# Kernel optimization log

Hardware: AMD Instinct MI355X
Metric: run time of the kernel (lower is better)

The kernel has to match this reference:

```python
import jax, jax.numpy as jnp
import numpy as np
from jax import lax

B, T_PAST, T_FUT, F_IN, F_OUT, H = 512, 128, 48, 64, 16, 512


def setup_inputs() -> dict:
    key = jax.random.key(0)
    ks = jax.random.split(key, 12)
    s = jnp.float32(0.05)
    p = lambda k, shape: jax.random.normal(k, shape, jnp.float32) * s
    return {
        "inp": jax.random.normal(ks[0], (B, T_PAST, F_IN), jnp.float32),
        "target_seq": jax.random.normal(ks[1], (B, T_FUT, F_OUT), jnp.float32),
        "enc1_Wk": p(ks[2], (F_IN, 4 * H)), "enc1_Wr": p(ks[3], (H, 4 * H)), "enc1_b": jnp.zeros((4 * H,), jnp.float32),
        "enc2_Wk": p(ks[4], (H, 4 * H)), "enc2_Wr": p(ks[5], (H, 4 * H)), "enc2_b": jnp.zeros((4 * H,), jnp.float32),
        "dec1_Wk": p(ks[6], (F_OUT, 4 * H)), "dec1_Wr": p(ks[7], (H, 4 * H)), "dec1_b": jnp.zeros((4 * H,), jnp.float32),
        "dec2_Wk": p(ks[8], (H, 4 * H)), "dec2_Wr": p(ks[9], (H, 4 * H)), "dec2_b": jnp.zeros((4 * H,), jnp.float32),
        "fc_W": p(ks[10], (H, F_OUT)), "fc_b": jnp.zeros((F_OUT,), jnp.float32),
    }


def _gates(z, c_prev):
    # Keras gate order: i, f, g(cell), o
    i, f, g, o = jnp.split(z, 4, axis=-1)
    c = jax.nn.sigmoid(f) * c_prev + jax.nn.sigmoid(i) * jnp.tanh(g)
    h = jax.nn.sigmoid(o) * jnp.tanh(c)
    return h, c


def _lstm_layer(xs, h0, c0, Wk, Wr, b):
    # xs: (B, T, D) -> (hs (B,T,H), hT, cT)
    xz = jnp.einsum("btd,dg->btg", xs, Wk) + b  # input projection precomputed
    def step(carry, xz_t):
        h, c = carry
        h2, c2 = _gates(xz_t + h @ Wr, c)
        return (h2, c2), h2
    (hT, cT), hs = lax.scan(step, (h0, c0), jnp.swapaxes(xz, 0, 1))
    return jnp.swapaxes(hs, 0, 1), hT, cT


def reference(inp, target_seq,
              enc1_Wk, enc1_Wr, enc1_b, enc2_Wk, enc2_Wr, enc2_b,
              dec1_Wk, dec1_Wr, dec1_b, dec2_Wk, dec2_Wr, dec2_b,
              fc_W, fc_b):
    b = inp.shape[0]
    z = jnp.zeros((b, H), inp.dtype)
    # Encoder: layer2 initial state = layer1 final state (as in source)
    h1s, h1, c1 = _lstm_layer(inp, z, z, enc1_Wk, enc1_Wr, enc1_b)
    _, h2, c2 = _lstm_layer(h1s, h1, c1, enc2_Wk, enc2_Wr, enc2_b)
    # Decoder: every future step restarts from (h2, c2) with teacher-forced
    # inputs -> steps are independent, compute all in parallel.
    z1 = (jnp.einsum("btf,fg->btg", target_seq, dec1_Wk)
          + (h2 @ dec1_Wr)[:, None, :] + dec1_b)          # (B, Tf, 4H)
    h1d, c1d = _gates(z1, c2[:, None, :])
    # layer2: input = h1d, initial state = (h1d, c1d) (chained per source)
    z2 = jnp.einsum("bth,hg->btg", h1d, dec2_Wk + dec2_Wr) + dec2_b
    h2d, _ = _gates(z2, c1d)
    return jnp.einsum("bth,hf->btf", h2d, fc_W) + fc_b    # (B, Tf, F_OUT)
```

## Files before the change

### kernel.cpp

```cpp
#include <hip/hip_runtime.h>


typedef _Float16 f16;
typedef _Float16 h8 __attribute__((ext_vector_type(8)));
typedef _Float16 h4 __attribute__((ext_vector_type(4)));
typedef float f32x4 __attribute__((ext_vector_type(4)));
typedef unsigned long long ull;

#define DEV static __device__ __forceinline__

constexpr int NB   = 512;
constexpr int TP   = 128;
constexpr int TFU  = 48;
constexpr int FIN  = 64;
constexpr int FOUT = 16;
constexpr int HS   = 512;
constexpr int G4   = 2048;

DEV float sigf(float x) { return 1.0f / (1.0f + __expf(-x)); }
DEV float tanh_(float x) { float e = __expf(2.0f * x); return 1.0f - 2.0f / (e + 1.0f); }

DEV void issue_ld(h8& d, const f16* p) {
  asm volatile("global_load_dwordx4 %0, %1, off" : "=v"(d) : "v"(p));
}
DEV void issue_ldc(h8& d, const f16* p) {
  asm volatile("global_load_dwordx4 %0, %1, off sc0 sc1" : "=v"(d) : "v"(p));
}
#define ILDX(dst, base, B) \
  asm volatile("global_load_dwordx4 %0, %1, off offset:" #B : "=v"(dst) : "v"(base));
#define ASM_VM0    asm volatile("s_waitcnt vmcnt(0)" ::: "memory")
#define ASM_VMC(N) asm volatile("s_waitcnt vmcnt(" #N ")" ::: "memory")
#define SBAR       __builtin_amdgcn_sched_barrier(0)

DEV void st_coh_h4(f16* p, h4 v) {
  union { h4 h; ull u; } c;
  c.h = v;
  __hip_atomic_store((ull*)p, c.u, __ATOMIC_RELAXED, __HIP_MEMORY_SCOPE_AGENT);
}

DEV unsigned xcc_id() {
  unsigned x;
  asm("s_getreg_b32 %0, hwreg(HW_REG_XCC_ID)" : "=s"(x));
  return x & 7;
}

DEV int ic2zc(int ic) { return ((ic >> 4) & 3) * 512 + ((ic >> 6) << 4) + (ic & 15); }

__global__ void k_conv(const float* __restrict__ a, const float* __restrict__ b,
                       f16* __restrict__ a16, f16* __restrict__ b16) {
  const size_t NA = (size_t)NB * TP * FIN;
  const size_t NBT = (size_t)NB * TFU * FOUT;
  for (size_t i = (size_t)blockIdx.x * blockDim.x + threadIdx.x; i < NA + NBT;
       i += (size_t)gridDim.x * blockDim.x) {
    if (i < NA) a16[i] = (f16)a[i];
    else        b16[i - NA] = (f16)b[i - NA];
  }
}

__global__ void k_bias(const float* __restrict__ b1, const float* __restrict__ b2,
                       const float* __restrict__ b3, const float* __restrict__ b4,
                       float* __restrict__ o1, float* __restrict__ o2,
                       float* __restrict__ o3, float* __restrict__ o4) {
  int ic = blockIdx.x * blockDim.x + threadIdx.x;
  if (ic < G4) {
    int zc = ic2zc(ic);
    o1[ic] = b1[zc]; o2[ic] = b2[zc]; o3[ic] = b3[zc]; o4[ic] = b4[zc];
  }
}

__global__ void k_pack(const float* __restrict__ A, const float* __restrict__ Bs,
                       int split, int NKC, int mode, f16* __restrict__ dst) {
  int i = blockIdx.x * blockDim.x + threadIdx.x;
  int total = 128 * NKC * 64;
  if (i >= total) return;
  int lane = i & 63, rem = i >> 6;
  int kc = rem % NKC, nt = rem / NKC;
  int zc = ic2zc(nt * 16 + (lane & 15));
  int k0 = kc * 32 + ((lane >> 4) << 3);
  h8 v;
#pragma unroll
  for (int j = 0; j < 8; j++) {
    int k = k0 + j;
    float x;
    if (mode == 2) x = A[(size_t)k * G4 + zc] + Bs[(size_t)k * G4 + zc];
    else x = (k < split) ? A[(size_t)k * G4 + zc] : Bs[(size_t)(k - split) * G4 + zc];
    v[j] = (f16)x;
  }
  *(h8*)(dst + (size_t)i * 8) = v;
}

__global__ void k_pack_dk16(const float* __restrict__ W, f16* __restrict__ dst) {
  int i = blockIdx.x * blockDim.x + threadIdx.x;
  if (i >= 128 * 64) return;
  int lane = i & 63, nt = i >> 6;
  int zc = ic2zc(nt * 16 + (lane & 15));
  h4 v;
#pragma unroll
  for (int j = 0; j < 4; j++) v[j] = (f16)W[(size_t)(((lane >> 4) << 2) + j) * G4 + zc];
  *(h4*)(dst + (size_t)i * 4) = v;
}

__global__ void k_pack_fc(const float* __restrict__ W, f16* __restrict__ dst) {
  int i = blockIdx.x * blockDim.x + threadIdx.x;
  if (i >= 32 * 64) return;
  int lane = i & 63, q = i >> 6;
  h4 v;
#pragma unroll
  for (int j = 0; j < 4; j++) {
    int k = q * 16 + ((lane >> 4) << 2) + j;
    v[j] = (f16)W[(size_t)k * FOUT + (lane & 15)];
  }
  *(h4*)(dst + (size_t)i * 4) = v;
}

template <int L, bool HIST>
__global__ __launch_bounds__(256, 1) void k_enc(
    const f16* __restrict__ wfrag, const float* __restrict__ biasI,
    f16* __restrict__ h1s, f16* __restrict__ h2r, f16* __restrict__ h2s,
    float* __restrict__ cT, const float* __restrict__ cInit,
    const f16* __restrict__ inp16, unsigned int* __restrict__ flags,
    int* __restrict__ roster) {
  constexpr int XKC = (L == 1) ? 2 : 16;
  constexpr int NKC = XKC + 16;
  constexpr size_t SLOT = (size_t)NB * HS;
  constexpr bool PLAIN_H = (L == 1) || HIST;

  extern __shared__ __align__(16) char smem[];
  f16* Bl = (f16*)smem;
  float* zl = (float*)(smem + (size_t)NKC * 4096);
  __shared__ int s_gc[2];

  const int tid = threadIdx.x, lane = tid & 63, wid = tid >> 6;
  const int wr = wid & 1, wc = wid >> 1;

  if (tid == 0) {
    unsigned x = xcc_id();
    int slot = atomicAdd(&roster[x], 1) & 31;
    s_gc[0] = (int)x; s_gc[1] = slot;
  }
  __syncthreads();
  const int g = s_gc[0], c = s_gc[1];
  const int b0 = g * 64;
  const int l15 = lane & 15, lk = (lane >> 4) << 3;
  const int trow = tid >> 2, tcol = (tid & 3) << 2;
  const int fbase = g * 32;

  {
    const uint4* src = (const uint4*)wfrag + (size_t)c * NKC * 256;
    uint4* dst = (uint4*)smem;
    for (int i = tid; i < NKC * 256; i += 256) dst[i] = src[i];
  }

  float bs[4][4];
#pragma unroll
  for (int ga = 0; ga < 4; ga++) {
    f32x4 bv = *(const f32x4*)(biasI + 64 * c + 16 * ga + tcol);
#pragma unroll
    for (int jj = 0; jj < 4; jj++) bs[ga][jj] = bv[jj];
  }

  float cst[4];
  if (L == 1) {
    cst[0] = cst[1] = cst[2] = cst[3] = 0.0f;
  } else {
    f32x4 cv = *(const f32x4*)(cInit + (size_t)(b0 + trow) * HS + 16 * c + tcol);
#pragma unroll
    for (int jj = 0; jj < 4; jj++) cst[jj] = cv[jj];
  }

  int arow[2];
#pragma unroll
  for (int m = 0; m < 2; m++) arow[m] = b0 + 32 * wr + 16 * m + l15;

  const f16* bbase[2];
#pragma unroll
  for (int n = 0; n < 2; n++) bbase[n] = Bl + ((size_t)(2 * wc + n) * NKC * 64 + lane) * 8;
  const f16* bh0 = bbase[0] + (size_t)XKC * 512;
  const f16* bh1 = bbase[1] + (size_t)XKC * 512;

  const size_t aoff0 = ((size_t)(lk >> 4) * 512 + arow[0]) * 16 + (lk & 8);
  const size_t aoff1 = ((size_t)(lk >> 4) * 512 + arow[1]) * 16 + (lk & 8);

  __syncthreads();

  for (int t = 0; t < TP; t++) {
    h8 ax0[XKC], ax1[XKC];
    if (L == 1) {
      const f16* xb0 = inp16 + ((size_t)arow[0] * TP + t) * FIN + lk;
      const f16* xb1 = inp16 + ((size_t)arow[1] * TP + t) * FIN + lk;
      ILDX(ax0[0], xb0, 0) ILDX(ax0[1], xb0, 64)
      ILDX(ax1[0], xb1, 0) ILDX(ax1[1], xb1, 64)
    } else {
      const f16* xb = h1s + (size_t)(t + 1) * SLOT;
      const f16* xp0 = xb + aoff0;
      const f16* xp1 = xb + aoff1;
#pragma unroll
      for (int kc = 0; kc < XKC; kc++) {
        issue_ld(ax0[kc], xp0);
        issue_ld(ax1[kc], xp1);
        xp0 += 16384; xp1 += 16384;
      }
    }

    if (t > 0) {
      if (wid == 0) {
        const unsigned int tgt = (unsigned int)t;
        for (;;) {
          unsigned int v = __hip_atomic_load(&flags[(size_t)(fbase + (lane & 31)) * 16],
                                             __ATOMIC_RELAXED, __HIP_MEMORY_SCOPE_AGENT);
          if (__all((int)(v >= tgt))) break;
          __builtin_amdgcn_s_sleep(1);
        }
      }
      __syncthreads();
    }
    ASM_VM0; SBAR;

    const f16* hb;
    if (L == 1) hb = h1s + (size_t)t * SLOT;
    else if (HIST) hb = (t == 0) ? (h1s + (size_t)TP * SLOT) : (h2s + (size_t)(t - 1) * SLOT);
    else hb = (t == 0) ? (h1s + (size_t)TP * SLOT) : (h2r + (size_t)((t - 1) & 1) * SLOT);
    const f16* hp0 = hb + aoff0;
    const f16* hp1 = hb + aoff1;

    h8 hA0[4], hA1[4], hB0[4], hB1[4];
#define LD_H(D, P) { if constexpr (PLAIN_H) issue_ld(D, P); else issue_ldc(D, P); }
#define HB_ISSUE(B0, B1)                                                       \
  {                                                                            \
    _Pragma("unroll") for (int j = 0; j < 4; j++) {                            \
      LD_H(B0[j], hp0)                                                         \
      LD_H(B1[j], hp1)                                                         \
      hp0 += 16384; hp1 += 16384;                                              \
    }                                                                          \
  }
#define HB_MFMA(B0, B1, KB)                                                    \
  {                                                                            \
    _Pragma("unroll") for (int j = 0; j < 4; j++) {                            \
      h8 bb0 = *(const h8*)(bh0 + (size_t)((KB) + j) * 512);                   \
      h8 bb1 = *(const h8*)(bh1 + (size_t)((KB) + j) * 512);                   \
      acc[0][0] = __builtin_amdgcn_mfma_f32_16x16x32_f16(B0[j], bb0, acc[0][0], 0, 0, 0); \
      acc[0][1] = __builtin_amdgcn_mfma_f32_16x16x32_f16(B0[j], bb1, acc[0][1], 0, 0, 0); \
      acc[1][0] = __builtin_amdgcn_mfma_f32_16x16x32_f16(B1[j], bb0, acc[1][0], 0, 0, 0); \
      acc[1][1] = __builtin_amdgcn_mfma_f32_16x16x32_f16(B1[j], bb1, acc[1][1], 0, 0, 0); \
    }                                                                          \
  }

    HB_ISSUE(hA0, hA1)
    HB_ISSUE(hB0, hB1)

    f32x4 acc[2][2] = {};

#pragma unroll
    for (int kc = 0; kc < XKC; kc++) {
      h8 bb0 = *(const h8*)(bbase[0] + (size_t)kc * 512);
      h8 bb1 = *(const h8*)(bbase[1] + (size_t)kc * 512);
      acc[0][0] = __builtin_amdgcn_mfma_f32_16x16x32_f16(ax0[kc], bb0, acc[0][0], 0, 0, 0);
      acc[0][1] = __builtin_amdgcn_mfma_f32_16x16x32_f16(ax0[kc], bb1, acc[0][1], 0, 0, 0);
      acc[1][0] = __builtin_amdgcn_mfma_f32_16x16x32_f16(ax1[kc], bb0, acc[1][0], 0, 0, 0);
      acc[1][1] = __builtin_amdgcn_mfma_f32_16x16x32_f16(ax1[kc], bb1, acc[1][1], 0, 0, 0);
    }

    ASM_VMC(8); SBAR;
    HB_MFMA(hA0, hA1, 0)
    HB_ISSUE(hA0, hA1)
    ASM_VMC(8); SBAR;
    HB_MFMA(hB0, hB1, 4)
    HB_ISSUE(hB0, hB1)
    ASM_VMC(8); SBAR;
    HB_MFMA(hA0, hA1, 8)
    ASM_VMC(0); SBAR;
    HB_MFMA(hB0, hB1, 12)
#undef HB_ISSUE
#undef HB_MFMA
#undef LD_H

#pragma unroll
    for (int m = 0; m < 2; m++)
#pragma unroll
      for (int n = 0; n < 2; n++) {
        int zr = 32 * wr + 16 * m + ((lane >> 4) << 2);
        int zc_ = 32 * wc + 16 * n + l15;
#pragma unroll
        for (int r = 0; r < 4; r++) zl[(size_t)(zr + r) * 65 + zc_] = acc[m][n][r];
      }
    __syncthreads();

    h4 hv;
#pragma unroll
    for (int jj = 0; jj < 4; jj++) {
      int hl = tcol + jj;
      float zi = zl[(size_t)trow * 65 + 0 + hl] + bs[0][jj];
      float zf = zl[(size_t)trow * 65 + 16 + hl] + bs[1][jj];
      float zg = zl[(size_t)trow * 65 + 32 + hl] + bs[2][jj];
      float zo = zl[(size_t)trow * 65 + 48 + hl] + bs[3][jj];
      float ci = sigf(zf) * cst[jj] + sigf(zi) * tanh_(zg);
      cst[jj] = ci;
      hv[jj] = (f16)(sigf(zo) * tanh_(ci));
    }
    {
      f16* hsl;
      if (L == 1) hsl = h1s + (size_t)(t + 1) * SLOT;
      else if (HIST) hsl = h2s + (size_t)t * SLOT;
      else hsl = h2r + (size_t)(t & 1) * SLOT;
      f16* hp = hsl + ((size_t)c * 512 + b0 + trow) * 16 + tcol;
      if constexpr (PLAIN_H) *(h4*)hp = hv;
      else st_coh_h4(hp, hv);
    }
    if (t == TP - 1) {
      f32x4 cp;
#pragma unroll
      for (int jj = 0; jj < 4; jj++) cp[jj] = cst[jj];
      *(f32x4*)(cT + (size_t)(b0 + trow) * HS + 16 * c + tcol) = cp;
    }

    ASM_VM0;
    __syncthreads();
    if (tid == 0)
      __hip_atomic_store(&flags[(size_t)(fbase + c) * 16], (unsigned int)(t + 1),
                         __ATOMIC_RELAXED, __HIP_MEMORY_SCOPE_AGENT);
  }
}

__global__ __launch_bounds__(256) void k_d1(const f16* __restrict__ h2T,
                                            const f16* __restrict__ wF,
                                            const float* __restrict__ bI,
                                            float* __restrict__ u) {
  const int tid = threadIdx.x, lane = tid & 63, wid = tid >> 6;
  const int wr = wid & 1, wc = wid >> 1;
  const int r0 = (blockIdx.x >> 4) * 32, ic0 = (blockIdx.x & 15) * 128;
  const int l15 = lane & 15, lk = (lane >> 4) << 3;
  const int arow = r0 + 16 * wr + l15;
  const f16* abase = h2T + ((size_t)(lk >> 4) * 512 + arow) * 16 + (lk & 8);
  const int nt0 = (ic0 >> 4) + 4 * wc;
  f32x4 acc[4] = {};
#pragma unroll
  for (int kc = 0; kc < 16; kc++) {
    h8 a = *(const h8*)(abase + (size_t)kc * 16384);
#pragma unroll
    for (int n = 0; n < 4; n++) {
      h8 b = *(const h8*)(wF + ((size_t)(nt0 + n) * 16 + kc) * 512 + (size_t)lane * 8);
      acc[n] = __builtin_amdgcn_mfma_f32_16x16x32_f16(a, b, acc[n], 0, 0, 0);
    }
  }
#pragma unroll
  for (int n = 0; n < 4; n++)
#pragma unroll
    for (int r = 0; r < 4; r++) {
      int row = r0 + 16 * wr + ((lane >> 4) << 2) + r;
      int ic = ic0 + 64 * wc + 16 * n + l15;
      u[(size_t)row * G4 + ic] = acc[n][r] + bI[ic];
    }
}

__global__ __launch_bounds__(256, 1) void k_d2(
    const f16* __restrict__ tg16, const f16* __restrict__ wk16F,
    const float* __restrict__ u, const float* __restrict__ c2T,
    const f16* __restrict__ w2F, const float* __restrict__ b2I,
    const f16* __restrict__ fcF, const float* __restrict__ fcb,
    float* __restrict__ out) {
  extern __shared__ __align__(16) char smem[];
  constexpr size_t H1OFF = 0;
  constexpr size_t C1OFF = 65536;
  constexpr size_t H2OFF = 131072;
  constexpr size_t RDOFF = 143360;

  const int tid = threadIdx.x, lane = tid & 63, wid = tid >> 6;
  const int l15 = lane & 15;
  const int r0 = blockIdx.x * 64;

  {
    const int wr = wid & 1, wc = wid >> 1;
    h4 a[2];
#pragma unroll
    for (int m = 0; m < 2; m++)
      a[m] = *(const h4*)(tg16 + (size_t)(r0 + 32 * wr + 16 * m + l15) * FOUT +
                          ((lane >> 4) << 2));
#pragma unroll 1
    for (int hc = 0; hc < 8; hc++) {
      f32x4 acc[2][8] = {};
#pragma unroll
      for (int n = 0; n < 8; n++) {
        int ntg = 16 * hc + 8 * wc + n;
        h4 b = *(const h4*)(wk16F + ((size_t)ntg * 64 + lane) * 4);
        acc[0][n] = __builtin_amdgcn_mfma_f32_16x16x16f16(a[0], b, acc[0][n], 0, 0, 0);
        acc[1][n] = __builtin_amdgcn_mfma_f32_16x16x16f16(a[1], b, acc[1][n], 0, 0, 0);
      }
#pragma unroll
      for (int m = 0; m < 2; m++)
#pragma unroll
        for (int s = 0; s < 2; s++) {
          int qq = 4 * hc + 2 * wc + s;
          int colh = 16 * qq + l15;
          int icb = 256 * hc + 128 * wc + 64 * s + l15;
#pragma unroll
          for (int r = 0; r < 4; r++) {
            int rl = 32 * wr + 16 * m + ((lane >> 4) << 2) + r;
            int grow = r0 + rl;
            int bidx = grow / 48;
            const float* ub = u + (size_t)bidx * G4;
            float zi = acc[m][4 * s + 0][r] + ub[icb];
            float zf = acc[m][4 * s + 1][r] + ub[icb + 16];
            float zg = acc[m][4 * s + 2][r] + ub[icb + 32];
            float zo = acc[m][4 * s + 3][r] + ub[icb + 48];
            float c2v = c2T[(size_t)bidx * HS + colh];
            float c1 = sigf(zf) * c2v + sigf(zi) * tanh_(zg);
            float h1 = sigf(zo) * tanh_(c1);
            size_t hb = (((size_t)rl * 1024) + (size_t)colh * 2) ^ (size_t)((rl & 7) << 4);
            *(f16*)(smem + H1OFF + hb) = (f16)h1;
            *(f16*)(smem + C1OFF + (size_t)rl * 1024 + (size_t)colh * 2) = (f16)c1;
          }
        }
    }
  }
  __syncthreads();

  {
    const int w = wid;
    f32x4 facc[4] = {};
#pragma unroll 1
    for (int sc = 0; sc < 8; sc++) {
      f32x4 acc[4][4] = {};
#pragma unroll
      for (int kc = 0; kc < 16; kc++) {
        h8 a[4];
#pragma unroll
        for (int mt = 0; mt < 4; mt++) {
          int rl = 16 * mt + l15;
          size_t ab = (((size_t)rl * 1024) + (size_t)(kc * 32 + ((lane >> 4) << 3)) * 2) ^
                      (size_t)((rl & 7) << 4);
          a[mt] = *(const h8*)(smem + H1OFF + ab);
        }
#pragma unroll
        for (int n = 0; n < 4; n++) {
          int nt = 32 * w + 4 * sc + n;
          h8 b = *(const h8*)(w2F + ((size_t)nt * 16 + kc) * 512 + (size_t)lane * 8);
#pragma unroll
          for (int mt = 0; mt < 4; mt++)
            acc[mt][n] = __builtin_amdgcn_mfma_f32_16x16x32_f16(a[mt], b, acc[mt][n], 0, 0, 0);
        }
      }
      int qq = 8 * w + sc;
#pragma unroll
      for (int mt = 0; mt < 4; mt++)
#pragma unroll
        for (int r = 0; r < 4; r++) {
          int rl = 16 * mt + ((lane >> 4) << 2) + r;
          int colh = 16 * qq + l15;
          int ic = 512 * w + 64 * sc + l15;
          float zi = acc[mt][0][r] + b2I[ic];
          float zf = acc[mt][1][r] + b2I[ic + 16];
          float zg = acc[mt][2][r] + b2I[ic + 32];
          float zo = acc[mt][3][r] + b2I[ic + 48];
          float c1v = (float)*(const f16*)(smem + C1OFF + (size_t)rl * 1024 + (size_t)colh * 2);
          float cn = sigf(zf) * c1v + sigf(zi) * tanh_(zg);
          float h2v = sigf(zo) * tanh_(cn);
          *(f16*)(smem + H2OFF + (size_t)w * 3072 + (size_t)rl * 48 + (size_t)l15 * 2) = (f16)h2v;
        }
#pragma unroll
      for (int mt = 0; mt < 4; mt++) {
        h4 aa = *(const h4*)(smem + H2OFF + (size_t)w * 3072 + (size_t)(16 * mt + l15) * 48 +
                             ((lane >> 4) << 3));
        h4 bb = *(const h4*)(fcF + ((size_t)qq * 64 + lane) * 4);
        facc[mt] = __builtin_amdgcn_mfma_f32_16x16x16f16(aa, bb, facc[mt], 0, 0, 0);
      }
    }
#pragma unroll
    for (int mt = 0; mt < 4; mt++)
#pragma unroll
      for (int r = 0; r < 4; r++) {
        int rl = 16 * mt + ((lane >> 4) << 2) + r;
        *(float*)(smem + RDOFF + ((size_t)w * 1152 + (size_t)rl * 18 + l15) * 4) = facc[mt][r];
      }
  }
  __syncthreads();

  {
    int rl = tid >> 2, c4 = (tid & 3) * 4;
    f32x4 o;
#pragma unroll
    for (int j = 0; j < 4; j++) {
      float s = 0.0f;
#pragma unroll
      for (int w = 0; w < 4; w++)
        s += *(const float*)(smem + RDOFF + ((size_t)w * 1152 + (size_t)rl * 18 + c4 + j) * 4);
      o[j] = s + fcb[c4 + j];
    }
    *(f32x4*)(out + (size_t)(r0 + rl) * FOUT + c4) = o;
  }
}

extern "C" void kernel_launch(void* const* d_in, const int* in_sizes, int n_in,
                              void* d_out, int out_size, void* d_ws, size_t ws_size,
                              hipStream_t stream) {
  const float* inp     = (const float*)d_in[0];
  const float* target  = (const float*)d_in[1];
  const float* e1Wk    = (const float*)d_in[2];
  const float* e1Wr    = (const float*)d_in[3];
  const float* e1b     = (const float*)d_in[4];
  const float* e2Wk    = (const float*)d_in[5];
  const float* e2Wr    = (const float*)d_in[6];
  const float* e2b     = (const float*)d_in[7];
  const float* d1Wk    = (const float*)d_in[8];
  const float* d1Wr    = (const float*)d_in[9];
  const float* d1b     = (const float*)d_in[10];
  const float* d2Wk    = (const float*)d_in[11];
  const float* d2Wr    = (const float*)d_in[12];
  const float* d2b     = (const float*)d_in[13];
  const float* fcW     = (const float*)d_in[14];
  const float* fcb     = (const float*)d_in[15];
  float* out = (float*)d_out;

  char* ws = (char*)d_ws;
  size_t off = 0;
  auto carve = [&](size_t bytes) { char* p = ws + off; off += bytes; return p; };
  f16*   inp16 = (f16*)carve((size_t)NB * TP * FIN * 2);
  f16*   tg16  = (f16*)carve((size_t)NB * TFU * FOUT * 2);
  f16*   h1s   = (f16*)carve((size_t)(TP + 1) * NB * HS * 2);
  f16*   h2r   = (f16*)carve((size_t)2 * NB * HS * 2);
  float* c1T   = (float*)carve((size_t)NB * HS * 4);
  float* c2T   = (float*)carve((size_t)NB * HS * 4);
  float* ubuf  = (float*)carve((size_t)NB * G4 * 4);
  f16*   Wc1F  = (f16*)carve((size_t)576 * G4 * 2);
  f16*   Wc2F  = (f16*)carve((size_t)1024 * G4 * 2);
  f16*   d1WrF = (f16*)carve((size_t)512 * G4 * 2);
  f16*   W2sF  = (f16*)carve((size_t)512 * G4 * 2);
  f16*   dk16F = (f16*)carve((size_t)16 * G4 * 2);
  f16*   fcWF  = (f16*)carve((size_t)512 * FOUT * 2);
  float* eB1I  = (float*)carve((size_t)G4 * 4);
  float* eB2I  = (float*)carve((size_t)G4 * 4);
  float* dB1I  = (float*)carve((size_t)G4 * 4);
  float* dB2I  = (float*)carve((size_t)G4 * 4);
  unsigned int* flags = (unsigned int*)carve(2 * 256 * 64);
  int*   roster = (int*)carve(256);
  const size_t H2S_BYTES = (size_t)TP * NB * HS * 2;
  bool hist = (ws_size >= off + H2S_BYTES);
  f16* h2s = hist ? (f16*)carve(H2S_BYTES) : nullptr;
  (void)n_in; (void)in_sizes; (void)out_size;

  constexpr int LDS_E1 = 18 * 4096 + 64 * 65 * 4;
  constexpr int LDS_E2 = 32 * 4096 + 64 * 65 * 4;
  constexpr int LDS_D2 = 143360 + 18432;
  {
    void (*p1)(const f16*, const float*, f16*, f16*, f16*, float*, const float*, const f16*,
               unsigned int*, int*) = k_enc<1, true>;
    void (*p2a)(const f16*, const float*, f16*, f16*, f16*, float*, const float*, const f16*,
                unsigned int*, int*) = k_enc<2, true>;
    void (*p2b)(const f16*, const float*, f16*, f16*, f16*, float*, const float*, const f16*,
                unsigned int*, int*) = k_enc<2, false>;
    hipFuncSetAttribute((const void*)p1, hipFuncAttributeMaxDynamicSharedMemorySize, LDS_E1);
    hipFuncSetAttribute((const void*)p2a, hipFuncAttributeMaxDynamicSharedMemorySize, LDS_E2);
    hipFuncSetAttribute((const void*)p2b, hipFuncAttributeMaxDynamicSharedMemorySize, LDS_E2);
    hipFuncSetAttribute((const void*)k_d2, hipFuncAttributeMaxDynamicSharedMemorySize, LDS_D2);
  }

  hipMemsetAsync(flags, 0, 2 * 256 * 64 + 256, stream);
  hipMemsetAsync(h1s, 0, (size_t)NB * HS * 2, stream);

  k_conv<<<4096, 256, 0, stream>>>(inp, target, inp16, tg16);
  k_bias<<<8, 256, 0, stream>>>(e1b, e2b, d1b, d2b, eB1I, eB2I, dB1I, dB2I);
  k_pack<<<576, 256, 0, stream>>>(e1Wk, e1Wr, 64, 18, 1, Wc1F);
  k_pack<<<1024, 256, 0, stream>>>(e2Wk, e2Wr, 512, 32, 1, Wc2F);
  k_pack<<<512, 256, 0, stream>>>(d1Wr, d1Wr, 512, 16, 1, d1WrF);
  k_pack<<<512, 256, 0, stream>>>(d2Wk, d2Wr, 0, 16, 2, W2sF);
  k_pack_dk16<<<32, 256, 0, stream>>>(d1Wk, dk16F);
  k_pack_fc<<<8, 256, 0, stream>>>(fcW, fcWF);

  k_enc<1, true><<<256, 256, LDS_E1, stream>>>(Wc1F, eB1I, h1s, h2r, h2s, c1T, nullptr,
                                               inp16, flags, roster);
  unsigned int* flags2 = flags + 256 * 16;
  int* roster2 = roster + 8;
  if (hist)
    k_enc<2, true><<<256, 256, LDS_E2, stream>>>(Wc2F, eB2I, h1s, h2r, h2s, c2T, c1T,
                                                 nullptr, flags2, roster2);
  else
    k_enc<2, false><<<256, 256, LDS_E2, stream>>>(Wc2F, eB2I, h1s, h2r, h2s, c2T, c1T,
                                                  nullptr, flags2, roster2);

  const f16* h2T = hist ? (h2s + (size_t)(TP - 1) * NB * HS) : (h2r + (size_t)1 * NB * HS);
  k_d1<<<256, 256, 0, stream>>>(h2T, d1WrF, dB1I, ubuf);
  k_d2<<<384, 256, LDS_D2, stream>>>(tg16, dk16F, ubuf, c2T, W2sF, dB2I, fcWF, fcb, out);
}
```

Before: 1.363 ms.

## Split recurrent step barrier into two partial waits with rotated K-chunk order

Each block now waits only for the producer blocks whose hidden-state chunks it consumes first, using a rotated K-chunk start so different blocks read different chunks first. It then waits for the rest midway through the recurrent matmul, overlapping synchronization latency with compute. All waves poll instead of only wave 0. The gate-staging LDS pitch changes from 65 to 68 so gate values can be read as float4 vectors, at the cost of possible bank conflicts on the scalar writes.

New measurement: 1.377 ms. About the same (+1.0%).

```diff
diff --git a/kernel.cpp b/kernel.cpp
--- a/kernel.cpp
+++ b/kernel.cpp
@@ -145,6 +145,11 @@
   const int trow = tid >> 2, tcol = (tid & 3) << 2;
   const int fbase = g * 32;
 
+  const int kc0 = ((c >> 1) + 1) & 15;
+  ull m1 = 0;
+  for (int i = 0; i < 8; i++) m1 |= (3ull << (2 * ((kc0 + i) & 15)));
+  const ull m2 = 0xFFFFFFFFull & ~m1;
+
   {
     const uint4* src = (const uint4*)wfrag + (size_t)c * NKC * 256;
     uint4* dst = (uint4*)smem;
@@ -182,6 +187,20 @@
   const size_t aoff1 = ((size_t)(lk >> 4) * 512 + arow[1]) * 16 + (lk & 8);
 
   __syncthreads();
+
+#define POLLW(MASK)                                                            \
+  {                                                                            \
+    const unsigned int tgt = (unsigned int)t;                                  \
+    for (;;) {                                                                 \
+      unsigned int v = __hip_atomic_load(                                      \
+          &flags[(size_t)(fbase + (lane & 31)) * 16], __ATOMIC_RELAXED,        \
+          __HIP_MEMORY_SCOPE_AGENT);                                           \
+      ull b = __ballot((int)(v >= tgt));                                       \
+      if ((b & (MASK)) == (MASK)) break;                                       \
+      __builtin_amdgcn_s_sleep(1);                                             \
+    }                                                                          \
+    SBAR;                                                                      \
+  }
 
   for (int t = 0; t < TP; t++) {
     h8 ax0[XKC], ax1[XKC];
@@ -202,42 +221,34 @@
       }
     }
 
-    if (t > 0) {
-      if (wid == 0) {
-        const unsigned int tgt = (unsigned int)t;
-        for (;;) {
-          unsigned int v = __hip_atomic_load(&flags[(size_t)(fbase + (lane & 31)) * 16],
-                                             __ATOMIC_RELAXED, __HIP_MEMORY_SCOPE_AGENT);
-          if (__all((int)(v >= tgt))) break;
-          __builtin_amdgcn_s_sleep(1);
-        }
-      }
-      __syncthreads();
-    }
+    if (t > 0) POLLW(m1);
     ASM_VM0; SBAR;
 
     const f16* hb;
     if (L == 1) hb = h1s + (size_t)t * SLOT;
     else if (HIST) hb = (t == 0) ? (h1s + (size_t)TP * SLOT) : (h2s + (size_t)(t - 1) * SLOT);
     else hb = (t == 0) ? (h1s + (size_t)TP * SLOT) : (h2r + (size_t)((t - 1) & 1) * SLOT);
-    const f16* hp0 = hb + aoff0;
-    const f16* hp1 = hb + aoff1;
+    const f16* hpb0 = hb + aoff0;
+    const f16* hpb1 = hb + aoff1;
 
     h8 hA0[4], hA1[4], hB0[4], hB1[4];
 #define LD_H(D, P) { if constexpr (PLAIN_H) issue_ld(D, P); else issue_ldc(D, P); }
-#define HB_ISSUE(B0, B1)                                                       \
+#define HB_ISSUE(B0, B1, P)                                                    \
   {                                                                            \
     _Pragma("unroll") for (int j = 0; j < 4; j++) {                            \
-      LD_H(B0[j], hp0)                                                         \
-      LD_H(B1[j], hp1)                                                         \
-      hp0 += 16384; hp1 += 16384;                                              \
+      int kk = (kc0 + (P) + j) & 15;                                           \
+      const f16* q0 = hpb0 + (size_t)kk * 16384;                               \
+      const f16* q1 = hpb1 + (size_t)kk * 16384;                               \
+      LD_H(B0[j], q0)                                                          \
+      LD_H(B1[j], q1)                                                          \
     }                                                                          \
   }
-#define HB_MFMA(B0, B1, KB)                                                    \
+#define HB_MFMA(B0, B1, P)                                                     \
   {                                                                            \
     _Pragma("unroll") for (int j = 0; j < 4; j++) {                            \
-      h8 bb0 = *(const h8*)(bh0 + (size_t)((KB) + j) * 512);                   \
-      h8 bb1 = *(const h8*)(bh1 + (size_t)((KB) + j) * 512);                   \
+      int kk = (kc0 + (P) + j) & 15;                                           \
+      h8 bb0 = *(const h8*)(bh0 + (size_t)kk * 512);                           \
+      h8 bb1 = *(const h8*)(bh1 + (size_t)kk * 512);                           \
       acc[0][0] = __builtin_amdgcn_mfma_f32_16x16x32_f16(B0[j], bb0, acc[0][0], 0, 0, 0); \
       acc[0][1] = __builtin_amdgcn_mfma_f32_16x16x32_f16(B0[j], bb1, acc[0][1], 0, 0, 0); \
       acc[1][0] = __builtin_amdgcn_mfma_f32_16x16x32_f16(B1[j], bb0, acc[1][0], 0, 0, 0); \
@@ -245,8 +256,8 @@
     }                                                                          \
   }
 
-    HB_ISSUE(hA0, hA1)
-    HB_ISSUE(hB0, hB1)
+    HB_ISSUE(hA0, hA1, 0)
+    HB_ISSUE(hB0, hB1, 4)
 
     f32x4 acc[2][2] = {};
 
@@ -262,10 +273,11 @@
 
     ASM_VMC(8); SBAR;
     HB_MFMA(hA0, hA1, 0)
-    HB_ISSUE(hA0, hA1)
+    if (t > 0) POLLW(m2);
+    HB_ISSUE(hA0, hA1, 8)
     ASM_VMC(8); SBAR;
     HB_MFMA(hB0, hB1, 4)
-    HB_ISSUE(hB0, hB1)
+    HB_ISSUE(hB0, hB1, 12)
     ASM_VMC(8); SBAR;
     HB_MFMA(hA0, hA1, 8)
     ASM_VMC(0); SBAR;
@@ -281,21 +293,27 @@
         int zr = 32 * wr + 16 * m + ((lane >> 4) << 2);
         int zc_ = 32 * wc + 16 * n + l15;
 #pragma unroll
-        for (int r = 0; r < 4; r++) zl[(size_t)(zr + r) * 65 + zc_] = acc[m][n][r];
+        for (int r = 0; r < 4; r++) zl[(size_t)(zr + r) * 68 + zc_] = acc[m][n][r];
       }
     __syncthreads();
 
     h4 hv;
-#pragma unroll
-    for (int jj = 0; jj < 4; jj++) {
-      int hl = tcol + jj;
-      float zi = zl[(size_t)trow * 65 + 0 + hl] + bs[0][jj];
-      float zf = zl[(size_t)trow * 65 + 16 + hl] + bs[1][jj];
-      float zg = zl[(size_t)trow * 65 + 32 + hl] + bs[2][jj];
-      float zo = zl[(size_t)trow * 65 + 48 + hl] + bs[3][jj];
-      float ci = sigf(zf) * cst[jj] + sigf(zi) * tanh_(zg);
-      cst[jj] = ci;
-      hv[jj] = (f16)(sigf(zo) * tanh_(ci));
+    {
+      const float* zrow = zl + (size_t)trow * 68 + tcol;
+      f32x4 z0 = *(const f32x4*)(zrow + 0);
+      f32x4 z1 = *(const f32x4*)(zrow + 16);
+      f32x4 z2 = *(const f32x4*)(zrow + 32);
+      f32x4 z3 = *(const f32x4*)(zrow + 48);
+#pragma unroll
+      for (int jj = 0; jj < 4; jj++) {
+        float zi = z0[jj] + bs[0][jj];
+        float zf = z1[jj] + bs[1][jj];
+        float zg = z2[jj] + bs[2][jj];
+        float zo = z3[jj] + bs[3][jj];
+        float ci = sigf(zf) * cst[jj] + sigf(zi) * tanh_(zg);
+        cst[jj] = ci;
+        hv[jj] = (f16)(sigf(zo) * tanh_(ci));
+      }
     }
     {
       f16* hsl;
@@ -319,6 +337,7 @@
       __hip_atomic_store(&flags[(size_t)(fbase + c) * 16], (unsigned int)(t + 1),
                          __ATOMIC_RELAXED, __HIP_MEMORY_SCOPE_AGENT);
   }
+#undef POLLW
 }
 
 __global__ __launch_bounds__(256) void k_d1(const f16* __restrict__ h2T,
@@ -537,8 +556,8 @@
   f16* h2s = hist ? (f16*)carve(H2S_BYTES) : nullptr;
   (void)n_in; (void)in_sizes; (void)out_size;
 
-  constexpr int LDS_E1 = 18 * 4096 + 64 * 65 * 4;
-  constexpr int LDS_E2 = 32 * 4096 + 64 * 65 * 4;
+  constexpr int LDS_E1 = 18 * 4096 + 64 * 68 * 4;
+  constexpr int LDS_E2 = 32 * 4096 + 64 * 68 * 4;
   constexpr int LDS_D2 = 143360 + 18432;
   {
     void (*p1)(const f16*, const float*, f16*, f16*, f16*, float*, const float*, const f16*,
```
